# Kernel tuning notes

Hardware: AMD Instinct MI355X
Metric: run time of the kernel (lower is better)

## Reference

```python
import jax, jax.numpy as jnp
import numpy as np

H = 512
L = 4096
LOC_CNT = 100000


def setup_inputs() -> dict:
    key = jax.random.key(0)
    ks = jax.random.split(key, 12)
    stdv = 1.0 / np.sqrt(H)

    def unif(k, shape):
        return jax.random.uniform(k, shape, dtype=jnp.float32, minval=-stdv, maxval=stdv)

    return {
        "td_upper": jax.random.uniform(ks[0], (L,), dtype=jnp.float32),
        "td_lower": jax.random.uniform(ks[1], (L,), dtype=jnp.float32),
        "ld_upper": jax.random.uniform(ks[2], (L,), dtype=jnp.float32),
        "ld_lower": jax.random.uniform(ks[3], (L,), dtype=jnp.float32),
        "loc": jax.random.randint(ks[4], (L,), 0, LOC_CNT, dtype=jnp.int64),
        "hx": jax.random.normal(ks[5], (H, 1), dtype=jnp.float32),
        "W_ih": unif(ks[6], (H, H)),
        "W_th_upper": unif(ks[7], (H, H)),
        "W_th_lower": unif(ks[8], (H, H)),
        "W_sh_upper": unif(ks[9], (H, H)),
        "W_sh_lower": unif(ks[10], (H, H)),
        "loc_table": unif(ks[11], (LOC_CNT, H)),
    }


def reference(td_upper, td_lower, ld_upper, ld_lower, loc, hx,
              W_ih, W_th_upper, W_th_lower, W_sh_upper, W_sh_lower, loc_table):
    # Gather location embeddings: (L, H)
    emb = loc_table[loc]
    # Ttd[i] @ emb[i] where Ttd[i] = (W_tu*tu_i + W_tl*tl_i)/(tu_i+tl_i):
    # distribute the scalar-weighted combine over the matmul.
    a = emb @ W_th_upper.T            # (L, H) == (W_th_upper @ emb[i])^T per row
    b = emb @ W_th_lower.T
    v = (a * td_upper[:, None] + b * td_lower[:, None]) / (td_upper + td_lower)[:, None]
    # Sld[i] @ v[i]
    c = v @ W_sh_upper.T
    d = v @ W_sh_lower.T
    w = (c * ld_upper[:, None] + d * ld_lower[:, None]) / (ld_upper + ld_lower)[:, None]
    # Original: torch.sum(torch.cat(...)) -> full scalar reduction over all L*H values.
    loc_vec = jnp.sum(w)
    usr_vec = W_ih @ hx               # (H, 1)
    return jax.nn.sigmoid(loc_vec + usr_vec)
```

## Files before the change

### kernel.cpp

```cpp
#include <hip/hip_runtime.h>
#include <math.h>

namespace {

constexpr int H = 512;
constexpr int L = 4096;

constexpr int WS_SU  = 0;
constexpr int WS_SL  = 512;
constexpr int WS_P   = 1024;
constexpr int WS_ACC = 3072;

__device__ inline float wave_reduce(float v) {
#pragma unroll
    for (int off = 32; off; off >>= 1) v += __shfl_xor(v, off, 64);
    return v;
}

__global__ void colsum_k(const float* __restrict__ Wsu,
                         const float* __restrict__ Wsl,
                         float* __restrict__ ws) {
    const int b = blockIdx.x;
    const int col = (b & 3) * 128 + threadIdx.x;
    const float* W = (b < 4) ? Wsu : Wsl;
    float acc = 0.f;
#pragma unroll 8
    for (int m = 0; m < H; ++m) acc += W[m * H + col];
    ws[((b < 4) ? WS_SU : WS_SL) + col] = acc;
    if (b == 0 && threadIdx.x == 0) ws[WS_ACC] = 0.f;
}

__global__ void pvec_k(const float* __restrict__ Wtu,
                       const float* __restrict__ Wtl,
                       float* __restrict__ ws) {
    const int v = blockIdx.x >> 2;
    const int j = (blockIdx.x & 3) * 128 + threadIdx.x;
    const float* s = ws + ((v < 2) ? WS_SU : WS_SL);
    const float* W = (v & 1) ? Wtl : Wtu;
    float acc = 0.f;
    for (int h = 0; h < H; ++h) acc += s[h] * W[h * H + j];
    ws[WS_P + v * H + j] = acc;
}

__global__ __launch_bounds__(512) void rowdot_k(
    const float* __restrict__ tu, const float* __restrict__ tl,
    const float* __restrict__ lu, const float* __restrict__ ll,
    const int* __restrict__ loc, const float* __restrict__ table,
    float* __restrict__ ws) {
    const int lane = threadIdx.x & 63;
    const int wid  = threadIdx.x >> 6;
    const int jA = lane * 4;
    const int jB = 256 + lane * 4;
    const float4* P = reinterpret_cast<const float4*>(ws + WS_P);
    const float4 puuA = P[(0 * H + jA) >> 2], puuB = P[(0 * H + jB) >> 2];
    const float4 pulA = P[(1 * H + jA) >> 2], pulB = P[(1 * H + jB) >> 2];
    const float4 pluA = P[(2 * H + jA) >> 2], pluB = P[(2 * H + jB) >> 2];
    const float4 pllA = P[(3 * H + jA) >> 2], pllB = P[(3 * H + jB) >> 2];

    float s_acc = 0.f;
    const int row0 = blockIdx.x * 32 + wid * 4;
#pragma unroll
    for (int r = 0; r < 4; ++r) {
        const int row = row0 + r;
        const float tuv = tu[row], tlv = tl[row];
        const float luv = lu[row], llv = ll[row];
        const float inv = 1.f / ((tuv + tlv) * (luv + llv));
        const float al = luv * tuv * inv;
        const float be = luv * tlv * inv;
        const float ga = llv * tuv * inv;
        const float de = llv * tlv * inv;
        const size_t base = (size_t)loc[row] * H;
        const float4 eA = *reinterpret_cast<const float4*>(table + base + jA);
        const float4 eB = *reinterpret_cast<const float4*>(table + base + jB);
        s_acc += eA.x * (al * puuA.x + be * pulA.x + ga * pluA.x + de * pllA.x);
        s_acc += eA.y * (al * puuA.y + be * pulA.y + ga * pluA.y + de * pllA.y);
        s_acc += eA.z * (al * puuA.z + be * pulA.z + ga * pluA.z + de * pllA.z);
        s_acc += eA.w * (al * puuA.w + be * pulA.w + ga * pluA.w + de * pllA.w);
        s_acc += eB.x * (al * puuB.x + be * pulB.x + ga * pluB.x + de * pllB.x);
        s_acc += eB.y * (al * puuB.y + be * pulB.y + ga * pluB.y + de * pllB.y);
        s_acc += eB.z * (al * puuB.z + be * pulB.z + ga * pluB.z + de * pllB.z);
        s_acc += eB.w * (al * puuB.w + be * pulB.w + ga * pluB.w + de * pllB.w);
    }
    s_acc = wave_reduce(s_acc);
    __shared__ float wpart[8];
    if (lane == 0) wpart[wid] = s_acc;
    __syncthreads();
    if (threadIdx.x == 0) {
        float t = 0.f;
#pragma unroll
        for (int w = 0; w < 8; ++w) t += wpart[w];
        atomicAdd(ws + WS_ACC, t);
    }
}

__global__ __launch_bounds__(256) void out_k(
    const float* __restrict__ Wih, const float* __restrict__ hx,
    const float* __restrict__ ws, float* __restrict__ out) {
    const int lane = threadIdx.x & 63;
    const int wid  = threadIdx.x >> 6;
    const int row  = blockIdx.x * 4 + wid;
    const int jA = lane * 4, jB = 256 + lane * 4;
    const float4 wA = *reinterpret_cast<const float4*>(Wih + row * H + jA);
    const float4 wB = *reinterpret_cast<const float4*>(Wih + row * H + jB);
    const float4 xA = *reinterpret_cast<const float4*>(hx + jA);
    const float4 xB = *reinterpret_cast<const float4*>(hx + jB);
    float acc = wA.x * xA.x + wA.y * xA.y + wA.z * xA.z + wA.w * xA.w
              + wB.x * xB.x + wB.y * xB.y + wB.z * xB.z + wB.w * xB.w;
    acc = wave_reduce(acc);
    if (lane == 0) {
        const float x = acc + ws[WS_ACC];
        out[row] = 1.f / (1.f + expf(-x));
    }
}

}

extern "C" void kernel_launch(void* const* d_in, const int* in_sizes, int n_in,
                              void* d_out, int out_size, void* d_ws, size_t ws_size,
                              hipStream_t stream) {
    const float* tu    = (const float*)d_in[0];
    const float* tl    = (const float*)d_in[1];
    const float* lu    = (const float*)d_in[2];
    const float* ll    = (const float*)d_in[3];
    const int*   loc   = (const int*)d_in[4];
    const float* hx    = (const float*)d_in[5];
    const float* Wih   = (const float*)d_in[6];
    const float* Wtu   = (const float*)d_in[7];
    const float* Wtl   = (const float*)d_in[8];
    const float* Wsu   = (const float*)d_in[9];
    const float* Wsl   = (const float*)d_in[10];
    const float* table = (const float*)d_in[11];
    float* ws  = (float*)d_ws;
    float* out = (float*)d_out;

    colsum_k<<<8, 128, 0, stream>>>(Wsu, Wsl, ws);
    pvec_k<<<16, 128, 0, stream>>>(Wtu, Wtl, ws);
    rowdot_k<<<128, 512, 0, stream>>>(tu, tl, lu, ll, loc, table, ws);
    out_k<<<128, 256, 0, stream>>>(Wih, hx, ws, out);
}
```

Measured before the change: 315.2 us.

## Reassociate computation to gather first and merge independent stages into one kernel

Changes the association order: the embedding gather is first reduced into four weighted column sums (g vectors), and only then contracted with the Wt matrices and the Ws column sums. This lets the gather, the Ws column sums and the W_ih matvec run as separate block ranges of one launch, instead of the old serial colsum and pvec kernels that used few blocks. The old pvec step had 16 blocks each walking a 512-long dependent chain, and it sat on the critical path. The cost is many float atomics into the workspace, a memset, and an extra small final kernel.

Measured after the change: 285.0 us. 9.6% less time.

```diff
diff --git a/kernel.cpp b/kernel.cpp
--- a/kernel.cpp
+++ b/kernel.cpp
@@ -8,8 +8,14 @@
 
 constexpr int WS_SU  = 0;
 constexpr int WS_SL  = 512;
-constexpr int WS_P   = 1024;
-constexpr int WS_ACC = 3072;
+constexpr int WS_G   = 1024;
+constexpr int WS_IHV = 3072;
+constexpr int WS_ACC = 3584;
+constexpr int WS_TOT = 3585;
+
+constexpr int GB = 256;
+constexpr int CB = 128;
+constexpr int WB = 8;
 
 __device__ inline float wave_reduce(float v) {
 #pragma unroll
@@ -17,100 +23,100 @@
     return v;
 }
 
-__global__ void colsum_k(const float* __restrict__ Wsu,
-                         const float* __restrict__ Wsl,
-                         float* __restrict__ ws) {
-    const int b = blockIdx.x;
-    const int col = (b & 3) * 128 + threadIdx.x;
-    const float* W = (b < 4) ? Wsu : Wsl;
-    float acc = 0.f;
-#pragma unroll 8
-    for (int m = 0; m < H; ++m) acc += W[m * H + col];
-    ws[((b < 4) ? WS_SU : WS_SL) + col] = acc;
-    if (b == 0 && threadIdx.x == 0) ws[WS_ACC] = 0.f;
-}
-
-__global__ void pvec_k(const float* __restrict__ Wtu,
-                       const float* __restrict__ Wtl,
-                       float* __restrict__ ws) {
-    const int v = blockIdx.x >> 2;
-    const int j = (blockIdx.x & 3) * 128 + threadIdx.x;
-    const float* s = ws + ((v < 2) ? WS_SU : WS_SL);
-    const float* W = (v & 1) ? Wtl : Wtu;
-    float acc = 0.f;
-    for (int h = 0; h < H; ++h) acc += s[h] * W[h * H + j];
-    ws[WS_P + v * H + j] = acc;
-}
-
-__global__ __launch_bounds__(512) void rowdot_k(
+__global__ __launch_bounds__(512) void stageA_k(
     const float* __restrict__ tu, const float* __restrict__ tl,
     const float* __restrict__ lu, const float* __restrict__ ll,
     const int* __restrict__ loc, const float* __restrict__ table,
+    const float* __restrict__ Wsu, const float* __restrict__ Wsl,
+    const float* __restrict__ Wih, const float* __restrict__ hx,
     float* __restrict__ ws) {
-    const int lane = threadIdx.x & 63;
-    const int wid  = threadIdx.x >> 6;
-    const int jA = lane * 4;
-    const int jB = 256 + lane * 4;
-    const float4* P = reinterpret_cast<const float4*>(ws + WS_P);
-    const float4 puuA = P[(0 * H + jA) >> 2], puuB = P[(0 * H + jB) >> 2];
-    const float4 pulA = P[(1 * H + jA) >> 2], pulB = P[(1 * H + jB) >> 2];
-    const float4 pluA = P[(2 * H + jA) >> 2], pluB = P[(2 * H + jB) >> 2];
-    const float4 pllA = P[(3 * H + jA) >> 2], pllB = P[(3 * H + jB) >> 2];
-
-    float s_acc = 0.f;
-    const int row0 = blockIdx.x * 32 + wid * 4;
+    const int b = blockIdx.x;
+    const int t = threadIdx.x;
+    if (b < GB) {
+        float aa = 0.f, ab = 0.f, ag = 0.f, ad = 0.f;
+        const int row0 = b * (L / GB);
 #pragma unroll
-    for (int r = 0; r < 4; ++r) {
-        const int row = row0 + r;
-        const float tuv = tu[row], tlv = tl[row];
-        const float luv = lu[row], llv = ll[row];
-        const float inv = 1.f / ((tuv + tlv) * (luv + llv));
-        const float al = luv * tuv * inv;
-        const float be = luv * tlv * inv;
-        const float ga = llv * tuv * inv;
-        const float de = llv * tlv * inv;
-        const size_t base = (size_t)loc[row] * H;
-        const float4 eA = *reinterpret_cast<const float4*>(table + base + jA);
-        const float4 eB = *reinterpret_cast<const float4*>(table + base + jB);
-        s_acc += eA.x * (al * puuA.x + be * pulA.x + ga * pluA.x + de * pllA.x);
-        s_acc += eA.y * (al * puuA.y + be * pulA.y + ga * pluA.y + de * pllA.y);
-        s_acc += eA.z * (al * puuA.z + be * pulA.z + ga * pluA.z + de * pllA.z);
-        s_acc += eA.w * (al * puuA.w + be * pulA.w + ga * pluA.w + de * pllA.w);
-        s_acc += eB.x * (al * puuB.x + be * pulB.x + ga * pluB.x + de * pllB.x);
-        s_acc += eB.y * (al * puuB.y + be * pulB.y + ga * pluB.y + de * pllB.y);
-        s_acc += eB.z * (al * puuB.z + be * pulB.z + ga * pluB.z + de * pllB.z);
-        s_acc += eB.w * (al * puuB.w + be * pulB.w + ga * pluB.w + de * pllB.w);
-    }
-    s_acc = wave_reduce(s_acc);
-    __shared__ float wpart[8];
-    if (lane == 0) wpart[wid] = s_acc;
-    __syncthreads();
-    if (threadIdx.x == 0) {
-        float t = 0.f;
+        for (int r = 0; r < L / GB; ++r) {
+            const int row = row0 + r;
+            const float tuv = tu[row], tlv = tl[row];
+            const float luv = lu[row], llv = ll[row];
+            const float ti = 1.f / (tuv + tlv), li = 1.f / (luv + llv);
+            const float Tu = tuv * ti, Tl = tlv * ti;
+            const float Lu = luv * li, Ll = llv * li;
+            const float e = table[(size_t)loc[row] * H + t];
+            aa += Lu * Tu * e;
+            ab += Lu * Tl * e;
+            ag += Ll * Tu * e;
+            ad += Ll * Tl * e;
+        }
+        atomicAdd(ws + WS_G + 0 * H + t, aa);
+        atomicAdd(ws + WS_G + 1 * H + t, ab);
+        atomicAdd(ws + WS_G + 2 * H + t, ag);
+        atomicAdd(ws + WS_G + 3 * H + t, ad);
+    } else if (b < GB + CB) {
+        const int cb = b - GB;
+        const int mat = cb >> 6;
+        const int m0 = (cb & 63) * (H / 64);
+        const float* W = mat ? Wsl : Wsu;
+        float acc = 0.f;
 #pragma unroll
-        for (int w = 0; w < 8; ++w) t += wpart[w];
-        atomicAdd(ws + WS_ACC, t);
+        for (int r = 0; r < H / 64; ++r) acc += W[(size_t)(m0 + r) * H + t];
+        atomicAdd(ws + (mat ? WS_SL : WS_SU) + t, acc);
+    } else {
+        const int wb = b - GB - CB;
+        const int lane = t & 63, wid = t >> 6;
+        const int j = lane * 8;
+        const float4 xA = *reinterpret_cast<const float4*>(hx + j);
+        const float4 xB = *reinterpret_cast<const float4*>(hx + j + 4);
+#pragma unroll
+        for (int r = 0; r < 8; ++r) {
+            const int row = wb * 64 + wid * 8 + r;
+            const float4 wA = *reinterpret_cast<const float4*>(Wih + (size_t)row * H + j);
+            const float4 wB = *reinterpret_cast<const float4*>(Wih + (size_t)row * H + j + 4);
+            float a = wA.x * xA.x + wA.y * xA.y + wA.z * xA.z + wA.w * xA.w
+                    + wB.x * xB.x + wB.y * xB.y + wB.z * xB.z + wB.w * xB.w;
+            a = wave_reduce(a);
+            if (lane == 0) ws[WS_IHV + row] = a;
+        }
     }
 }
 
-__global__ __launch_bounds__(256) void out_k(
-    const float* __restrict__ Wih, const float* __restrict__ hx,
+__global__ __launch_bounds__(512) void stageB_k(
+    const float* __restrict__ Wtu, const float* __restrict__ Wtl,
+    float* __restrict__ ws) {
+    const int t = threadIdx.x;
+    const int lane = t & 63, wid = t >> 6;
+    const int gw = blockIdx.x * 8 + wid;
+    const int mat = gw >> 9;
+    const int h = gw & (H - 1);
+    const float* W = mat ? Wtl : Wtu;
+    const float* g1 = ws + WS_G + (mat ? 1 : 0) * H;
+    const float* g2 = ws + WS_G + (mat ? 3 : 2) * H;
+    const float suh = ws[WS_SU + h], slh = ws[WS_SL + h];
+    const int j = lane * 8;
+    const float4 wA = *reinterpret_cast<const float4*>(W + (size_t)h * H + j);
+    const float4 wB = *reinterpret_cast<const float4*>(W + (size_t)h * H + j + 4);
+    const float4 aA = *reinterpret_cast<const float4*>(g1 + j);
+    const float4 aB = *reinterpret_cast<const float4*>(g1 + j + 4);
+    const float4 bA = *reinterpret_cast<const float4*>(g2 + j);
+    const float4 bB = *reinterpret_cast<const float4*>(g2 + j + 4);
+    float acc = wA.x * (suh * aA.x + slh * bA.x)
+              + wA.y * (suh * aA.y + slh * bA.y)
+              + wA.z * (suh * aA.z + slh * bA.z)
+              + wA.w * (suh * aA.w + slh * bA.w)
+              + wB.x * (suh * aB.x + slh * bB.x)
+              + wB.y * (suh * aB.y + slh * bB.y)
+              + wB.z * (suh * aB.z + slh * bB.z)
+              + wB.w * (suh * aB.w + slh * bB.w);
+    acc = wave_reduce(acc);
+    if (lane == 0) atomicAdd(ws + WS_ACC, acc);
+}
+
+__global__ __launch_bounds__(512) void stageC_k(
     const float* __restrict__ ws, float* __restrict__ out) {
-    const int lane = threadIdx.x & 63;
-    const int wid  = threadIdx.x >> 6;
-    const int row  = blockIdx.x * 4 + wid;
-    const int jA = lane * 4, jB = 256 + lane * 4;
-    const float4 wA = *reinterpret_cast<const float4*>(Wih + row * H + jA);
-    const float4 wB = *reinterpret_cast<const float4*>(Wih + row * H + jB);
-    const float4 xA = *reinterpret_cast<const float4*>(hx + jA);
-    const float4 xB = *reinterpret_cast<const float4*>(hx + jB);
-    float acc = wA.x * xA.x + wA.y * xA.y + wA.z * xA.z + wA.w * xA.w
-              + wB.x * xB.x + wB.y * xB.y + wB.z * xB.z + wB.w * xB.w;
-    acc = wave_reduce(acc);
-    if (lane == 0) {
-        const float x = acc + ws[WS_ACC];
-        out[row] = 1.f / (1.f + expf(-x));
-    }
+    const int t = threadIdx.x;
+    const float x = ws[WS_ACC] + ws[WS_IHV + t];
+    out[t] = 1.f / (1.f + expf(-x));
 }
 
 }
@@ -133,8 +139,9 @@
     float* ws  = (float*)d_ws;
     float* out = (float*)d_out;
 
-    colsum_k<<<8, 128, 0, stream>>>(Wsu, Wsl, ws);
-    pvec_k<<<16, 128, 0, stream>>>(Wtu, Wtl, ws);
-    rowdot_k<<<128, 512, 0, stream>>>(tu, tl, lu, ll, loc, table, ws);
-    out_k<<<128, 256, 0, stream>>>(Wih, hx, ws, out);
+    hipMemsetAsync(ws, 0, WS_TOT * sizeof(float), stream);
+    stageA_k<<<GB + CB + WB, 512, 0, stream>>>(tu, tl, lu, ll, loc, table,
+                                               Wsu, Wsl, Wih, hx, ws);
+    stageB_k<<<128, 512, 0, stream>>>(Wtu, Wtl, ws);
+    stageC_k<<<1, 512, 0, stream>>>(ws, out);
 }
```
